# Kernel optimization log

Measured on AMD Instinct MI355X. Metric: run time of the kernel, lower is better.

Reference implementation:

```python
import jax, jax.numpy as jnp
import numpy as np

C = 128  # in_dim

def _proj(x, w, b):
    # 1x1 conv: x [b,c,h,w], w [out,in], b [out] -> [b,out,h*w]
    bsz, c, h, wd = x.shape
    y = jnp.einsum('bchw,oc->bohw', x, w) + b[None, :, None, None]
    return y.reshape(bsz, -1, h * wd)

def setup_inputs() -> dict:
    key = jax.random.key(0)
    ks = jax.random.split(key, 7)
    x = jax.random.normal(ks[0], (16, C, 128, 128), dtype=jnp.float32)
    s = 1.0 / np.sqrt(C)
    qw = jax.random.normal(ks[1], (C, C), dtype=jnp.float32) * s
    kw = jax.random.normal(ks[2], (C, C), dtype=jnp.float32) * s
    vw = jax.random.normal(ks[3], (C, C), dtype=jnp.float32) * s
    qb = jax.random.normal(ks[4], (C,), dtype=jnp.float32) * 0.01
    kb = jax.random.normal(ks[5], (C,), dtype=jnp.float32) * 0.01
    vb = jax.random.normal(ks[6], (C,), dtype=jnp.float32) * 0.01
    return {'x': x, 'qw': qw, 'qb': qb, 'kw': kw, 'kb': kb, 'vw': vw, 'vb': vb}

def reference(x, qw, qb, kw, kb, vw, vb):
    x_s, x_t = jnp.split(x, 2, axis=0)
    b, c, h, w = x_s.shape
    q_s = _proj(x_s, qw, qb); q_t = _proj(x_t, qw, qb)   # [b,c,N]
    k_s = _proj(x_s, kw, kb); k_t = _proj(x_t, kw, kb)   # [b,c,N]
    v_s = _proj(x_s, vw, vb); v_t = _proj(x_t, vw, vb)   # [b,c,N]
    # channel cross-attentions: contract over spatial N -> [b,c,c]
    a_st = jax.nn.softmax(jnp.einsum('bcn,bdn->bcd', q_t, k_s), axis=-1)
    a_ts = jax.nn.softmax(jnp.einsum('bcn,bdn->bcd', q_s, k_t), axis=-1)
    att = jax.nn.softmax(jnp.einsum('bce,bde->bcd', a_st, a_ts), axis=-1)
    out_s = jnp.einsum('bcd,bdn->bcn', att, v_s).reshape(b, c, h, w)
    out_t = jnp.einsum('bcd,bdn->bcn', att, v_t).reshape(b, c, h, w)
    return jnp.concatenate((x_s + out_s, x_t + out_t), axis=0)
```

## Files before the change

### kernel.cpp

```cpp
#include <hip/hip_runtime.h>
#include <hip/hip_bf16.h>

#define CC 128
#define NSP 16384
#define NFULL (CC * NSP)

typedef float f32x4 __attribute__((ext_vector_type(4)));
typedef short s16x8 __attribute__((ext_vector_type(8)));
typedef unsigned int u32x4 __attribute__((ext_vector_type(4)));

#define GLOAD16(g, l) __builtin_amdgcn_global_load_lds( \
    (const __attribute__((address_space(1))) void*)(g), \
    (__attribute__((address_space(3))) void*)(l), 16, 0, 0)

__device__ __forceinline__ unsigned bf16rne(float f) {
  unsigned u = __float_as_uint(f);
  return ((u + 0x7FFFu + ((u >> 16) & 1u)) >> 16) & 0xFFFFu;
}

__device__ __forceinline__ uint2 packpair(float x0, float x1) {
  __hip_bfloat162 h2 = __float22bfloat162_rn(make_float2(x0, x1));
  unsigned hu = *reinterpret_cast<unsigned*>(&h2);
  float hf0 = __uint_as_float(hu << 16);
  float hf1 = __uint_as_float(hu & 0xFFFF0000u);
  __hip_bfloat162 l2 = __float22bfloat162_rn(make_float2(x0 - hf0, x1 - hf1));
  unsigned lu = *reinterpret_cast<unsigned*>(&l2);
  return make_uint2(hu, lu);
}

__global__ __launch_bounds__(256) void zerok(float* __restrict__ p, int n) {
  int i = blockIdx.x * 256 + threadIdx.x;
  if (i < n) p[i] = 0.f;
}

__global__ __launch_bounds__(256, 2) void k1_mfma(const float* __restrict__ x,
    float* __restrict__ Mdst, float* __restrict__ rs, float* __restrict__ rt,
    float* __restrict__ rspart, float* __restrict__ rtpart,
    int nst, int mode) {
  const int b = blockIdx.y;
  const int chunk = blockIdx.x;
  const int n0 = chunk * (nst * 32);
  const int t = threadIdx.x;
  const int w = t >> 6, l = t & 63;
  const int wr = w >> 1, wc = w & 1;
  const int lr = l & 15, lg = l >> 4;
  __shared__ __align__(16) char LB[2][2][128 * 128];
  const float* Xs = x + (size_t)b * NFULL;
  const float* Xt = x + (size_t)(b + 8) * NFULL;
  const int srow0 = w * 32 + (l >> 3);
  const int sn16x = (l & 7);

  f32x4 acc[4][4];
#pragma unroll
  for (int a = 0; a < 4; ++a)
#pragma unroll
    for (int bb = 0; bb < 4; ++bb) acc[a][bb] = (f32x4){0.f, 0.f, 0.f, 0.f};
  float rtp[4] = {0.f, 0.f, 0.f, 0.f};
  float rsp[4] = {0.f, 0.f, 0.f, 0.f};

  {
#pragma unroll
    for (int i = 0; i < 4; ++i) {
      int row = srow0 + i * 8;
      int n16 = sn16x ^ (row & 7);
      GLOAD16(Xt + (size_t)row * NSP + n0 + n16 * 4, &LB[0][0][(w * 32 + i * 8) * 128]);
      GLOAD16(Xs + (size_t)row * NSP + n0 + n16 * 4, &LB[0][1][(w * 32 + i * 8) * 128]);
    }
  }

  for (int s = 0; s < nst; ++s) {
    const int cur = s & 1;
    __syncthreads();
    if (s + 1 < nst) {
      const int nb = n0 + (s + 1) * 32;
#pragma unroll
      for (int i = 0; i < 4; ++i) {
        int row = srow0 + i * 8;
        int n16 = sn16x ^ (row & 7);
        GLOAD16(Xt + (size_t)row * NSP + nb + n16 * 4, &LB[cur ^ 1][0][(w * 32 + i * 8) * 128]);
        GLOAD16(Xs + (size_t)row * NSP + nb + n16 * 4, &LB[cur ^ 1][1][(w * 32 + i * 8) * 128]);
      }
    }
    const char* A = &LB[cur][0][0];
    const char* B = &LB[cur][1][0];
    s16x8 ah[4], al[4], bh[4], bl[4];
#pragma unroll
    for (int a = 0; a < 4; ++a) {
      int row = wr * 64 + a * 16 + lr;
      int base = row * 128, sw = row & 7;
      f32x4 f0 = *(const f32x4*)(A + base + (((lg * 2) ^ sw) << 4));
      f32x4 f1 = *(const f32x4*)(A + base + (((lg * 2 + 1) ^ sw) << 4));
      rtp[a] += ((f0[0] + f0[1]) + (f0[2] + f0[3])) + ((f1[0] + f1[1]) + (f1[2] + f1[3]));
      uint2 p0 = packpair(f0[0], f0[1]);
      uint2 p1 = packpair(f0[2], f0[3]);
      uint2 p2 = packpair(f1[0], f1[1]);
      uint2 p3 = packpair(f1[2], f1[3]);
      u32x4 H = {p0.x, p1.x, p2.x, p3.x};
      u32x4 L = {p0.y, p1.y, p2.y, p3.y};
      ah[a] = __builtin_bit_cast(s16x8, H);
      al[a] = __builtin_bit_cast(s16x8, L);
    }
#pragma unroll
    for (int bb = 0; bb < 4; ++bb) {
      int row = wc * 64 + bb * 16 + lr;
      int base = row * 128, sw = row & 7;
      f32x4 f0 = *(const f32x4*)(B + base + (((lg * 2) ^ sw) << 4));
      f32x4 f1 = *(const f32x4*)(B + base + (((lg * 2 + 1) ^ sw) << 4));
      rsp[bb] += ((f0[0] + f0[1]) + (f0[2] + f0[3])) + ((f1[0] + f1[1]) + (f1[2] + f1[3]));
      uint2 p0 = packpair(f0[0], f0[1]);
      uint2 p1 = packpair(f0[2], f0[3]);
      uint2 p2 = packpair(f1[0], f1[1]);
      uint2 p3 = packpair(f1[2], f1[3]);
      u32x4 H = {p0.x, p1.x, p2.x, p3.x};
      u32x4 L = {p0.y, p1.y, p2.y, p3.y};
      bh[bb] = __builtin_bit_cast(s16x8, H);
      bl[bb] = __builtin_bit_cast(s16x8, L);
    }
#pragma unroll
    for (int a = 0; a < 4; ++a)
#pragma unroll
      for (int bb = 0; bb < 4; ++bb) {
        acc[a][bb] = __builtin_amdgcn_mfma_f32_16x16x32_bf16(ah[a], bh[bb], acc[a][bb], 0, 0, 0);
        acc[a][bb] = __builtin_amdgcn_mfma_f32_16x16x32_bf16(ah[a], bl[bb], acc[a][bb], 0, 0, 0);
        acc[a][bb] = __builtin_amdgcn_mfma_f32_16x16x32_bf16(al[a], bh[bb], acc[a][bb], 0, 0, 0);
      }
  }

#pragma unroll
  for (int a = 0; a < 4; ++a) {
    float vt = rtp[a];
    vt += __shfl_xor(vt, 16);
    vt += __shfl_xor(vt, 32);
    float vs = rsp[a];
    vs += __shfl_xor(vs, 16);
    vs += __shfl_xor(vs, 32);
    if (l < 16) {
      if (wc == 0) {
        int row = wr * 64 + a * 16 + l;
        if (mode == 0) rtpart[((size_t)chunk * 8 + b) * CC + row] = vt;
        else atomicAdd(&rt[b * CC + row], vt);
      }
      if (wr == 0) {
        int row = wc * 64 + a * 16 + l;
        if (mode == 0) rspart[((size_t)chunk * 8 + b) * CC + row] = vs;
        else atomicAdd(&rs[b * CC + row], vs);
      }
    }
  }

  const int rquad = lg << 2;
  if (mode == 0) {
    float* Mp = Mdst + ((size_t)chunk * 8 + b) * (CC * CC);
#pragma unroll
    for (int a = 0; a < 4; ++a)
#pragma unroll
      for (int bb = 0; bb < 4; ++bb)
#pragma unroll
        for (int r = 0; r < 4; ++r) {
          int i = wr * 64 + a * 16 + rquad + r;
          int j = wc * 64 + bb * 16 + lr;
          Mp[i * CC + j] = acc[a][bb][r];
        }
  } else {
    float* Mp = Mdst + (size_t)b * (CC * CC);
#pragma unroll
    for (int a = 0; a < 4; ++a)
#pragma unroll
      for (int bb = 0; bb < 4; ++bb)
#pragma unroll
        for (int r = 0; r < 4; ++r) {
          int i = wr * 64 + a * 16 + rquad + r;
          int j = wc * 64 + bb * 16 + lr;
          atomicAdd(&Mp[i * CC + j], acc[a][bb][r]);
        }
  }
}

__global__ __launch_bounds__(256) void k1_reduce(const float* __restrict__ Mpart,
    const float* __restrict__ rspart, const float* __restrict__ rtpart,
    float* __restrict__ M, float* __restrict__ rs, float* __restrict__ rt,
    int NB) {
  const int t = threadIdx.x;
  if (blockIdx.x < 128) {
    const int i4 = blockIdx.x * 256 + t;
    const int b = i4 >> 12;
    const int e = (i4 & 4095) * 4;
    f32x4 s = (f32x4){0.f, 0.f, 0.f, 0.f};
    for (int c = 0; c < NB; ++c) {
      f32x4 v = *(const f32x4*)(Mpart + ((size_t)c * 8 + b) * (CC * CC) + e);
      s += v;
    }
    *(f32x4*)(M + (size_t)b * CC * CC + e) = s;
  } else if (blockIdx.x == 128) {
    const int e = t * 4;
    f32x4 s = (f32x4){0.f, 0.f, 0.f, 0.f};
    for (int c = 0; c < NB; ++c) s += *(const f32x4*)(rtpart + (size_t)c * 1024 + e);
    *(f32x4*)(rt + e) = s;
  } else {
    const int e = t * 4;
    f32x4 s = (f32x4){0.f, 0.f, 0.f, 0.f};
    for (int c = 0; c < NB; ++c) s += *(const f32x4*)(rspart + (size_t)c * 1024 + e);
    *(f32x4*)(rs + e) = s;
  }
}

__global__ __launch_bounds__(256) void k2ab(const float* __restrict__ M,
    const float* __restrict__ qw, const float* __restrict__ kw,
    const float* __restrict__ qb, const float* __restrict__ kb,
    const float* __restrict__ rs, const float* __restrict__ rt,
    float* __restrict__ Ast, float* __restrict__ Ats) {
  const int b = blockIdx.y;
  const int c0 = blockIdx.x * 4;
  __shared__ float Big[128][132];
  __shared__ float Wq[4][128];
  __shared__ float T12[2][4][128];
  __shared__ float uvv[2][4];
  __shared__ float wv2[2][128];
  const int t = threadIdx.x;
  const float* Mb = M + (size_t)b * CC * CC;
#pragma unroll
  for (int p = 0; p < 16; ++p) {
    int f = p * 256 + t;
    int row = f >> 5, c4 = (f & 31) * 4;
    *(f32x4*)&Big[row][c4] = *(const f32x4*)(Mb + row * CC + c4);
  }
  if (t < 128) {
    int row = t >> 5, c4 = (t & 31) * 4;
    *(f32x4*)&Wq[row][c4] = *(const f32x4*)(qw + (c0 + row) * CC + c4);
  }
  __syncthreads();
  if (t < 8) {
    int c = t & 3;
    const float* r = ((t < 4) ? rs : rt) + b * CC;
    float s = 0.f;
    for (int i = 0; i < CC; ++i) s += Wq[c][i] * r[i];
    uvv[(t < 4) ? 1 : 0][c] = s;
  }
  const int tr = t >> 6;
  const int L = t & 63;
  {
    float a1[2] = {0.f, 0.f}, a2[2] = {0.f, 0.f};
    for (int i = 0; i < CC; ++i) {
      float wq = Wq[tr][i];
#pragma unroll
      for (int j = 0; j < 2; ++j) a1[j] += wq * Big[i][L + 64 * j];
    }
    for (int i4 = 0; i4 < 32; ++i4) {
      f32x4 wq4 = *(const f32x4*)&Wq[tr][i4 * 4];
#pragma unroll
      for (int j = 0; j < 2; ++j) {
        f32x4 m4 = *(const f32x4*)&Big[L + 64 * j][i4 * 4];
        a2[j] += wq4[0]*m4[0] + wq4[1]*m4[1] + wq4[2]*m4[2] + wq4[3]*m4[3];
      }
    }
#pragma unroll
    for (int j = 0; j < 2; ++j) {
      T12[0][tr][L + 64 * j] = a1[j];
      T12[1][tr][L + 64 * j] = a2[j];
    }
  }
  __syncthreads();
#pragma unroll
  for (int p = 0; p < 16; ++p) {
    int f = p * 256 + t;
    int row = f >> 5, c4 = (f & 31) * 4;
    *(f32x4*)&Big[row][c4] = *(const f32x4*)(kw + row * CC + c4);
  }
  __syncthreads();
  {
    int d = t & 127, wh = t >> 7;
    const float* r = (wh ? rt : rs) + b * CC;
    float s = 0.f;
    for (int i4 = 0; i4 < 32; ++i4) {
      f32x4 w4 = *(const f32x4*)&Big[d][i4 * 4];
      s += w4[0]*r[i4*4] + w4[1]*r[i4*4+1] + w4[2]*r[i4*4+2] + w4[3]*r[i4*4+3];
    }
    wv2[wh][d] = s;
  }
  __syncthreads();
  const int c = c0 + tr;
  const float bqc = qb[c];
#pragma unroll 1
  for (int which = 0; which < 2; ++which) {
    float g[2];
#pragma unroll
    for (int j = 0; j < 2; ++j) {
      int d = L + 64 * j;
      g[j] = uvv[which][tr] * kb[d] + bqc * wv2[which][d] + 16384.f * bqc * kb[d];
    }
    for (int j4 = 0; j4 < 32; ++j4) {
      f32x4 tv4 = *(const f32x4*)&T12[which][tr][j4 * 4];
#pragma unroll
      for (int j = 0; j < 2; ++j) {
        f32x4 w4 = *(const f32x4*)&Big[L + 64 * j][j4 * 4];
        g[j] += tv4[0]*w4[0] + tv4[1]*w4[1] + tv4[2]*w4[2] + tv4[3]*w4[3];
      }
    }
    float m = fmaxf(g[0], g[1]);
#pragma unroll
    for (int off = 1; off < 64; off <<= 1) m = fmaxf(m, __shfl_xor(m, off));
    float s = g[0] = expf(g[0] - m);
    s += (g[1] = expf(g[1] - m));
#pragma unroll
    for (int off = 1; off < 64; off <<= 1) s += __shfl_xor(s, off);
    const float inv = 1.f / s;
    float* A = (which ? Ats : Ast) + (size_t)b * CC * CC + (size_t)c * CC;
    A[L] = g[0] * inv;
    A[L + 64] = g[1] * inv;
  }
}

__global__ __launch_bounds__(256) void k2cd(const float* __restrict__ Ast,
    const float* __restrict__ Ats, const float* __restrict__ vw,
    const float* __restrict__ vb, unsigned short* __restrict__ Pbf,
    float* __restrict__ c0v) {
  const int b = blockIdx.y;
  const int c0 = blockIdx.x * 4;
  __shared__ float Big[128][132];
  __shared__ float Tl[4][128];
  __shared__ float Al[4][128];
  const int t = threadIdx.x;
  const float* Bb = Ats + (size_t)b * CC * CC;
  const float* Tb = Ast + (size_t)b * CC * CC;
#pragma unroll
  for (int p = 0; p < 16; ++p) {
    int f = p * 256 + t;
    int row = f >> 5, c4 = (f & 31) * 4;
    *(f32x4*)&Big[row][c4] = *(const f32x4*)(Bb + row * CC + c4);
  }
  if (t < 128) {
    int row = t >> 5, c4 = (t & 31) * 4;
    *(f32x4*)&Tl[row][c4] = *(const f32x4*)(Tb + (c0 + row) * CC + c4);
  }
  __syncthreads();
  const int tr = t >> 6;
  const int L = t & 63;
  {
    float g[2] = {0.f, 0.f};
    for (int e4 = 0; e4 < 32; ++e4) {
      f32x4 tv4 = *(const f32x4*)&Tl[tr][e4 * 4];
#pragma unroll
      for (int j = 0; j < 2; ++j) {
        f32x4 a4 = *(const f32x4*)&Big[L + 64 * j][e4 * 4];
        g[j] += tv4[0]*a4[0] + tv4[1]*a4[1] + tv4[2]*a4[2] + tv4[3]*a4[3];
      }
    }
    float m = fmaxf(g[0], g[1]);
#pragma unroll
    for (int off = 1; off < 64; off <<= 1) m = fmaxf(m, __shfl_xor(m, off));
    float s = g[0] = expf(g[0] - m);
    s += (g[1] = expf(g[1] - m));
#pragma unroll
    for (int off = 1; off < 64; off <<= 1) s += __shfl_xor(s, off);
    const float inv = 1.f / s;
    Al[tr][L] = g[0] * inv;
    Al[tr][L + 64] = g[1] * inv;
  }
  __syncthreads();
#pragma unroll
  for (int p = 0; p < 16; ++p) {
    int f = p * 256 + t;
    int row = f >> 5, c4 = (f & 31) * 4;
    *(f32x4*)&Big[row][c4] = *(const f32x4*)(vw + row * CC + c4);
  }
  __syncthreads();
  float p2[2] = {0.f, 0.f};
  for (int d = 0; d < CC; ++d) {
    float av = Al[tr][d];
#pragma unroll
    for (int j = 0; j < 2; ++j) p2[j] += av * Big[d][L + 64 * j];
  }
  float csum = Al[tr][L] * vb[L] + Al[tr][L + 64] * vb[L + 64];
#pragma unroll
  for (int off = 1; off < 64; off <<= 1) csum += __shfl_xor(csum, off);
  const int c = c0 + tr;
  if ((c & 63) == L) p2[c >> 6] += 1.0f;
  unsigned short* Pp = Pbf + (size_t)b * CC * CC + (size_t)c * CC;
  Pp[L] = (unsigned short)bf16rne(p2[0]);
  Pp[L + 64] = (unsigned short)bf16rne(p2[1]);
  if (L == 0) c0v[b * CC + c] = csum;
}

__global__ __launch_bounds__(256, 2) void k3_mfma(const float* __restrict__ x,
    const unsigned short* __restrict__ Pbf, const float* __restrict__ c0v,
    float* __restrict__ out) {
  const int im = blockIdx.y;
  const int pb = im & 7;
  const int n0 = blockIdx.x * 256;
  const float* X = x + (size_t)im * NFULL;
  float* O = out + (size_t)im * NFULL;
  __shared__ unsigned short XT[256 * 128];
  __shared__ float c0l[128];
  const int t = threadIdx.x;
  const int w = t >> 6, l = t & 63;
  const int ln = l & 15, lg = l >> 4;
  if (t < 128) c0l[t] = c0v[pb * CC + t];
#pragma unroll
  for (int p = 0; p < 16; ++p) {
    int d0 = 2 * (t >> 4) + 32 * (p & 3);
    int n4 = (t & 15) * 4 + 64 * (p >> 2);
    f32x4 x0 = *(const f32x4*)(X + (size_t)d0 * NSP + n0 + n4);
    f32x4 x1 = *(const f32x4*)(X + (size_t)(d0 + 1) * NSP + n0 + n4);
#pragma unroll
    for (int i = 0; i < 4; ++i) {
      int n = n4 + i;
      __hip_bfloat162 h2 = __float22bfloat162_rn(make_float2(x0[i], x1[i]));
      unsigned pk = *reinterpret_cast<unsigned*>(&h2);
      int g = ((((n & 3) << 1) ^ ((n >> 2) & 7)) << 4);
      int off = (n * 256 + d0 * 2) ^ g;
      *(unsigned*)((char*)XT + off) = pk;
    }
  }
  const unsigned short* Pg0 = Pbf + (size_t)pb * (CC * CC) + (size_t)ln * CC + lg * 8;
  s16x8 Af0[4][4];
#pragma unroll
  for (int a = 0; a < 4; ++a)
#pragma unroll
    for (int kk = 0; kk < 4; ++kk)
      Af0[a][kk] = *(const s16x8*)(Pg0 + a * 16 * CC + kk * 32);
  __syncthreads();

#pragma unroll
  for (int h = 0; h < 2; ++h) {
    s16x8 Af[4][4];
    if (h == 0) {
#pragma unroll
      for (int a = 0; a < 4; ++a)
#pragma unroll
        for (int kk = 0; kk < 4; ++kk) Af[a][kk] = Af0[a][kk];
    } else {
      const unsigned short* Pg = Pg0 + (size_t)64 * CC;
#pragma unroll
      for (int a = 0; a < 4; ++a)
#pragma unroll
        for (int kk = 0; kk < 4; ++kk)
          Af[a][kk] = *(const s16x8*)(Pg + a * 16 * CC + kk * 32);
    }
#pragma unroll
    for (int sub = 0; sub < 4; ++sub) {
      int row = sub * 64 + w * 16 + ln;
      int g = ((((row & 3) << 1) ^ ((row >> 2) & 7)) << 4);
      s16x8 bf[4];
#pragma unroll
      for (int kk = 0; kk < 4; ++kk)
        bf[kk] = *(const s16x8*)((char*)XT + ((row * 256 + kk * 64 + lg * 16) ^ g));
      f32x4 acc[4];
#pragma unroll
      for (int a = 0; a < 4; ++a) acc[a] = (f32x4){0.f, 0.f, 0.f, 0.f};
#pragma unroll
      for (int kk = 0; kk < 4; ++kk)
#pragma unroll
        for (int a = 0; a < 4; ++a)
          acc[a] = __builtin_amdgcn_mfma_f32_16x16x32_bf16(bf[kk], Af[a][kk], acc[a], 0, 0, 0);
      int nbase = n0 + sub * 64 + w * 16 + lg * 4;
#pragma unroll
      for (int a = 0; a < 4; ++a) {
        int c = h * 64 + a * 16 + ln;
        float cc0 = c0l[c];
        f32x4 r = acc[a];
        r[0] += cc0; r[1] += cc0; r[2] += cc0; r[3] += cc0;
        __builtin_nontemporal_store(r, (f32x4*)(O + (size_t)c * NSP + nbase));
      }
    }
  }
}

extern "C" void kernel_launch(void* const* d_in, const int* in_sizes, int n_in,
                              void* d_out, int out_size, void* d_ws, size_t ws_size,
                              hipStream_t stream) {
  (void)in_sizes; (void)n_in; (void)out_size;
  const float* x  = (const float*)d_in[0];
  const float* qw = (const float*)d_in[1];
  const float* qb = (const float*)d_in[2];
  const float* kw = (const float*)d_in[3];
  const float* kb = (const float*)d_in[4];
  const float* vw = (const float*)d_in[5];
  const float* vb = (const float*)d_in[6];
  float* out = (float*)d_out;
  float* ws = (float*)d_ws;
  float* M   = ws;
  float* rs  = M + 131072;
  float* rt  = rs + 1024;
  float* AST = rt + 1024;
  float* ATS = AST + 131072;
  unsigned short* Pbf = (unsigned short*)(ATS + 131072);
  float* c0v = ATS + 131072 + 65536;
  float* Mpart = c0v + 1024;
  const size_t base_floats = (size_t)(Mpart - ws);

  int NB, mode;
  if (ws_size >= (base_floats + (size_t)32 * (131072 + 2048)) * 4) { NB = 32; mode = 0; }
  else { NB = 32; mode = 1; }
  const int nst = (16384 / NB) / 32;
  float* rtpart = Mpart + (size_t)NB * 131072;
  float* rspart = rtpart + (size_t)NB * 1024;

  if (mode == 1) zerok<<<(133120 + 255) / 256, 256, 0, stream>>>(M, 133120);
  k1_mfma<<<dim3(NB, 8), 256, 0, stream>>>(x, mode ? M : Mpart, rs, rt,
                                           rspart, rtpart, nst, mode);
  if (mode == 0)
    k1_reduce<<<130, 256, 0, stream>>>(Mpart, rspart, rtpart, M, rs, rt, NB);
  k2ab<<<dim3(32, 8), 256, 0, stream>>>(M, qw, kw, qb, kb, rs, rt, AST, ATS);
  k2cd<<<dim3(32, 8), 256, 0, stream>>>(AST, ATS, vw, vb, Pbf, c0v);
  k3_mfma<<<dim3(64, 16), 256, 0, stream>>>(x, Pbf, c0v, out);
}
```

Baseline: 125.7 us.

## Process two spatial tiles per k3 block, prefetching second tile into registers

Each k3_mfma block now handles 512 spatial positions instead of 256, with half as many blocks in the grid. After staging the first tile, the block loads and converts the second tile's x values into registers while it computes and stores the first tile, then writes them to LDS for a second pass. This aims to hide global load latency behind MFMA and store work and to amortise the P and c0 setup. In exchange it uses 64 extra VGPRs per thread, which may cut occupancy under launch_bounds(256,2), and it leaves fewer blocks to fill the GPU.

Result: slower. 149.1 us (+18.6%).

```diff
diff --git a/kernel.cpp b/kernel.cpp
--- a/kernel.cpp
+++ b/kernel.cpp
@@ -386,7 +386,7 @@
     float* __restrict__ out) {
   const int im = blockIdx.y;
   const int pb = im & 7;
-  const int n0 = blockIdx.x * 256;
+  const int n00 = blockIdx.x * 512;
   const float* X = x + (size_t)im * NFULL;
   float* O = out + (size_t)im * NFULL;
   __shared__ unsigned short XT[256 * 128];
@@ -395,20 +395,20 @@
   const int w = t >> 6, l = t & 63;
   const int ln = l & 15, lg = l >> 4;
   if (t < 128) c0l[t] = c0v[pb * CC + t];
+
 #pragma unroll
   for (int p = 0; p < 16; ++p) {
     int d0 = 2 * (t >> 4) + 32 * (p & 3);
     int n4 = (t & 15) * 4 + 64 * (p >> 2);
-    f32x4 x0 = *(const f32x4*)(X + (size_t)d0 * NSP + n0 + n4);
-    f32x4 x1 = *(const f32x4*)(X + (size_t)(d0 + 1) * NSP + n0 + n4);
+    f32x4 x0 = *(const f32x4*)(X + (size_t)d0 * NSP + n00 + n4);
+    f32x4 x1 = *(const f32x4*)(X + (size_t)(d0 + 1) * NSP + n00 + n4);
 #pragma unroll
     for (int i = 0; i < 4; ++i) {
       int n = n4 + i;
       __hip_bfloat162 h2 = __float22bfloat162_rn(make_float2(x0[i], x1[i]));
       unsigned pk = *reinterpret_cast<unsigned*>(&h2);
       int g = ((((n & 3) << 1) ^ ((n >> 2) & 7)) << 4);
-      int off = (n * 256 + d0 * 2) ^ g;
-      *(unsigned*)((char*)XT + off) = pk;
+      *(unsigned*)((char*)XT + ((n * 256 + d0 * 2) ^ g)) = pk;
     }
   }
   const unsigned short* Pg0 = Pbf + (size_t)pb * (CC * CC) + (size_t)ln * CC + lg * 8;
@@ -419,6 +419,20 @@
     for (int kk = 0; kk < 4; ++kk)
       Af0[a][kk] = *(const s16x8*)(Pg0 + a * 16 * CC + kk * 32);
   __syncthreads();
+
+  u32x4 pk1[16];
+#pragma unroll
+  for (int p = 0; p < 16; ++p) {
+    int d0 = 2 * (t >> 4) + 32 * (p & 3);
+    int n4 = (t & 15) * 4 + 64 * (p >> 2);
+    f32x4 x0 = *(const f32x4*)(X + (size_t)d0 * NSP + n00 + 256 + n4);
+    f32x4 x1 = *(const f32x4*)(X + (size_t)(d0 + 1) * NSP + n00 + 256 + n4);
+#pragma unroll
+    for (int i = 0; i < 4; ++i) {
+      __hip_bfloat162 h2 = __float22bfloat162_rn(make_float2(x0[i], x1[i]));
+      pk1[p][i] = *reinterpret_cast<unsigned*>(&h2);
+    }
+  }
 
 #pragma unroll
   for (int h = 0; h < 2; ++h) {
@@ -452,7 +466,65 @@
 #pragma unroll
         for (int a = 0; a < 4; ++a)
           acc[a] = __builtin_amdgcn_mfma_f32_16x16x32_bf16(bf[kk], Af[a][kk], acc[a], 0, 0, 0);
-      int nbase = n0 + sub * 64 + w * 16 + lg * 4;
+      int nbase = n00 + sub * 64 + w * 16 + lg * 4;
+#pragma unroll
+      for (int a = 0; a < 4; ++a) {
+        int c = h * 64 + a * 16 + ln;
+        float cc0 = c0l[c];
+        f32x4 r = acc[a];
+        r[0] += cc0; r[1] += cc0; r[2] += cc0; r[3] += cc0;
+        __builtin_nontemporal_store(r, (f32x4*)(O + (size_t)c * NSP + nbase));
+      }
+    }
+  }
+
+  __syncthreads();
+#pragma unroll
+  for (int p = 0; p < 16; ++p) {
+    int d0 = 2 * (t >> 4) + 32 * (p & 3);
+    int n4 = (t & 15) * 4 + 64 * (p >> 2);
+#pragma unroll
+    for (int i = 0; i < 4; ++i) {
+      int n = n4 + i;
+      int g = ((((n & 3) << 1) ^ ((n >> 2) & 7)) << 4);
+      *(unsigned*)((char*)XT + ((n * 256 + d0 * 2) ^ g)) = pk1[p][i];
+    }
+  }
+  __syncthreads();
+
+#pragma unroll
+  for (int h = 0; h < 2; ++h) {
+    s16x8 Af[4][4];
+    if (h == 0) {
+#pragma unroll
+      for (int a = 0; a < 4; ++a)
+#pragma unroll
+        for (int kk = 0; kk < 4; ++kk) Af[a][kk] = Af0[a][kk];
+    } else {
+      const unsigned short* Pg = Pg0 + (size_t)64 * CC;
+#pragma unroll
+      for (int a = 0; a < 4; ++a)
+#pragma unroll
+        for (int kk = 0; kk < 4; ++kk)
+          Af[a][kk] = *(const s16x8*)(Pg + a * 16 * CC + kk * 32);
+    }
+#pragma unroll
+    for (int sub = 0; sub < 4; ++sub) {
+      int row = sub * 64 + w * 16 + ln;
+      int g = ((((row & 3) << 1) ^ ((row >> 2) & 7)) << 4);
+      s16x8 bf[4];
+#pragma unroll
+      for (int kk = 0; kk < 4; ++kk)
+        bf[kk] = *(const s16x8*)((char*)XT + ((row * 256 + kk * 64 + lg * 16) ^ g));
+      f32x4 acc[4];
+#pragma unroll
+      for (int a = 0; a < 4; ++a) acc[a] = (f32x4){0.f, 0.f, 0.f, 0.f};
+#pragma unroll
+      for (int kk = 0; kk < 4; ++kk)
+#pragma unroll
+        for (int a = 0; a < 4; ++a)
+          acc[a] = __builtin_amdgcn_mfma_f32_16x16x32_bf16(bf[kk], Af[a][kk], acc[a], 0, 0, 0);
+      int nbase = n00 + 256 + sub * 64 + w * 16 + lg * 4;
 #pragma unroll
       for (int a = 0; a < 4; ++a) {
         int c = h * 64 + a * 16 + ln;
@@ -502,5 +574,5 @@
     k1_reduce<<<130, 256, 0, stream>>>(Mpart, rspart, rtpart, M, rs, rt, NB);
   k2ab<<<dim3(32, 8), 256, 0, stream>>>(M, qw, kw, qb, kb, rs, rt, AST, ATS);
   k2cd<<<dim3(32, 8), 256, 0, stream>>>(AST, ATS, vw, vb, Pbf, c0v);
-  k3_mfma<<<dim3(64, 16), 256, 0, stream>>>(x, Pbf, c0v, out);
-}
+  k3_mfma<<<dim3(32, 16), 256, 0, stream>>>(x, Pbf, c0v, out);
+}
```
